# Kernel tuning notes

Hardware: AMD Instinct MI355X
Metric: run time of the kernel (lower is better)

The kernel has to match this reference:

```python
import jax, jax.numpy as jnp
import numpy as np

B, S, E, A = 4, 2048, 1024, 1024

def setup_inputs() -> dict:
    key = jax.random.key(0)
    ks = jax.random.split(key, 6)
    scale = 1.0 / np.sqrt(E)
    return {
        "query": jax.random.normal(ks[0], (B, S, E), jnp.float32),
        "key": jax.random.normal(ks[1], (B, S, E), jnp.float32),
        "value": jax.random.normal(ks[2], (B, S, E), jnp.float32),
        "Wq": jax.random.normal(ks[3], (E, A), jnp.float32) * scale,
        "bq": jnp.zeros((A,), jnp.float32),
        "Wk": jax.random.normal(ks[4], (E, A), jnp.float32) * scale,
        "bk": jnp.zeros((A,), jnp.float32),
        "Wv": jax.random.normal(ks[5], (E, A), jnp.float32) * scale,
        "bv": jnp.zeros((A,), jnp.float32),
    }

def reference(query, key, value, Wq, bq, Wk, bk, Wv, bv):
    # QKV linear projections: [B,S,E] @ [E,A] + [A]
    q = jnp.einsum("bse,ea->bsa", query, Wq) + bq
    k = jnp.einsum("bse,ea->bsa", key, Wk) + bk
    v = jnp.einsum("bse,ea->bsa", value, Wv) + bv
    # scaled dot-product attention (no mask, single head)
    inv_sqrt_d = 1.0 / jnp.sqrt(jnp.asarray(A, q.dtype))
    scores = jnp.einsum("bqa,bka->bqk", q, k) * inv_sqrt_d  # [B,S,S]
    probs = jax.nn.softmax(scores, axis=-1)
    return jnp.einsum("bqk,bka->bqa", probs, v)
```

## Files before the change

### kernel.cpp

```cpp
#include <hip/hip_runtime.h>

typedef unsigned short u16;
typedef __attribute__((ext_vector_type(4))) float f32x4;
typedef __attribute__((ext_vector_type(8))) short s16x8;
typedef __attribute__((ext_vector_type(8))) unsigned short u16x8;
typedef __attribute__((ext_vector_type(4))) unsigned short u16x4;

__device__ __forceinline__ u16 f2b(float x) {
  union { float f; unsigned u; } v; v.f = x;
  unsigned r = v.u + 0x7fffu + ((v.u >> 16) & 1u);
  return (u16)(r >> 16);
}
__device__ __forceinline__ float b2f(u16 x) {
  union { unsigned u; float f; } v; v.u = ((unsigned)x) << 16;
  return v.f;
}

__global__ __launch_bounds__(256) void cast3_f32_bf16(const float* __restrict__ s0,
                                                      const float* __restrict__ s1,
                                                      const float* __restrict__ s2,
                                                      u16* __restrict__ dst, long n4) {
  const float* src = (blockIdx.y == 0) ? s0 : ((blockIdx.y == 1) ? s1 : s2);
  long i = blockIdx.x * 256 + threadIdx.x;
  if (i >= n4) return;
  float4 f = ((const float4*)src)[i];
  u16x4 o;
  o.x = f2b(f.x); o.y = f2b(f.y); o.z = f2b(f.z); o.w = f2b(f.w);
  ((u16x4*)(dst + blockIdx.y * n4 * 4))[i] = o;
}

__global__ __launch_bounds__(256) void transpose_cast_w3(const float* __restrict__ w0,
                                                         const float* __restrict__ w1,
                                                         const float* __restrict__ w2,
                                                         u16* __restrict__ Wt, int E_, int A_) {
  __shared__ float tile[32][33];
  const float* W = (blockIdx.z == 0) ? w0 : ((blockIdx.z == 1) ? w1 : w2);
  u16* dst = Wt + (long)blockIdx.z * E_ * A_;
  int a0 = blockIdx.x * 32, e0 = blockIdx.y * 32;
  int tx = threadIdx.x & 31, ty = threadIdx.x >> 5;
  for (int i = ty; i < 32; i += 8) tile[i][tx] = W[(long)(e0 + i) * A_ + a0 + tx];
  __syncthreads();
  for (int i = ty; i < 32; i += 8) dst[(long)(a0 + i) * E_ + e0 + tx] = f2b(tile[tx][i]);
}

template<int BN, bool OUT_BF16>
__global__ __launch_bounds__(512, 2)
void gemmK32(const u16* __restrict__ Ag, const u16* __restrict__ Bg,
             const float* __restrict__ b0, const float* __restrict__ b1,
             const float* __restrict__ b2, void* __restrict__ Cg,
             int gn, int K, int N, float scale,
             long sA, long sB, long sC,
             u16* __restrict__ VtG, long vtB, int vtS) {
  constexpr int J = BN / 64;
  constexpr int WN = BN / 4;
  constexpr int OPS = 2 + BN / 128;
  constexpr int BUFSZ = (256 + BN) * 64;
  __shared__ __align__(128) char ldsc[4 * BUFSZ];

  const int t = threadIdx.x;
  const int w = t >> 6, l = t & 63;
  const int wm = w >> 2, wn = w & 3;

  const int nwg = gridDim.x;
  const int Lb = blockIdx.x;
  const int chunk = nwg >> 3;
  const int id = (Lb & 7) * chunk + (Lb >> 3);
  const int im = id / gn, in = id % gn;
  const int m0 = im * 256, n0 = in * BN;
  const int z = blockIdx.z;
  const float* bias = (z == 0) ? b0 : ((z == 1) ? b1 : b2);

  const u16* Ab = Ag + (long)z * sA + (long)m0 * K;
  const u16* Bb = Bg + (long)z * sB + (long)n0 * K;

  const long so0 = (long)(t >> 2) * K + (long)(((t & 3) ^ ((t >> 3) & 3)) << 3);
  const int d16 = t * 16;

  const int cbR = ((l >> 4) ^ ((l >> 1) & 3)) << 4;
  const int aB = (wm << 13) + ((l & 15) << 6) + cbR;
  const int bB = 16384 + wn * (WN * 64) + ((l & 15) << 6) + cbR;

  f32x4 acc[8][J] = {};
  s16x8 af[4], bf[J];
  const int NTt = K >> 5;

#define GLD(SRC, DST)                                                                        \
  __builtin_amdgcn_global_load_lds(                                                         \
      (const __attribute__((address_space(1))) unsigned int*)(SRC),                         \
      (__attribute__((address_space(3))) unsigned int*)(DST), 16, 0, 0)

#define STGA(TT) do {                                                                        \
    const u16* _s = Ab + ((long)(TT) << 5) + so0;                                            \
    char* _d = ldsc + ((TT) & 3) * BUFSZ + d16;                                              \
    GLD(_s, _d);                                                                             \
    GLD(_s + (long)128 * K, _d + 8192);                                                      \
  } while (0)

#define STGB(TT) do {                                                                        \
    const u16* _s = Bb + ((long)(TT) << 5) + so0;                                            \
    char* _d = ldsc + ((TT) & 3) * BUFSZ + 16384 + d16;                                      \
    GLD(_s, _d);                                                                             \
    if (BN == 256) GLD(_s + (long)128 * K, _d + 8192);                                       \
  } while (0)

  STGA(0); STGB(0); STGA(1); STGB(1); STGA(2); STGB(2);
  if (OPS == 4) asm volatile("s_waitcnt vmcnt(8)" ::: "memory");
  else          asm volatile("s_waitcnt vmcnt(6)" ::: "memory");
  __builtin_amdgcn_s_barrier();

  for (int tt = 0; tt < NTt; ++tt) {
    const int base = (tt & 3) * BUFSZ;
#pragma unroll
    for (int i = 0; i < 4; ++i) af[i] = *(const s16x8*)(ldsc + base + aB + (i << 10));
#pragma unroll
    for (int j = 0; j < J; ++j) bf[j] = *(const s16x8*)(ldsc + base + bB + (j << 10));
    if (tt + 3 < NTt) STGA(tt + 3);
    __builtin_amdgcn_s_setprio(1);
#pragma unroll
    for (int i = 0; i < 4; ++i)
#pragma unroll
      for (int j = 0; j < J; ++j)
        acc[i][j] = __builtin_amdgcn_mfma_f32_16x16x32_bf16(af[i], bf[j], acc[i][j], 0, 0, 0);
    __builtin_amdgcn_s_setprio(0);
    __builtin_amdgcn_s_barrier();

#pragma unroll
    for (int i = 0; i < 4; ++i) af[i] = *(const s16x8*)(ldsc + base + aB + 4096 + (i << 10));
    if (tt + 3 < NTt) STGB(tt + 3);
    __builtin_amdgcn_s_setprio(1);
#pragma unroll
    for (int i = 0; i < 4; ++i)
#pragma unroll
      for (int j = 0; j < J; ++j)
        acc[4 + i][j] = __builtin_amdgcn_mfma_f32_16x16x32_bf16(af[i], bf[j], acc[4 + i][j], 0, 0, 0);
    __builtin_amdgcn_s_setprio(0);
    if (tt <= NTt - 4) {
      if (OPS == 4) asm volatile("s_waitcnt vmcnt(8)" ::: "memory");
      else          asm volatile("s_waitcnt vmcnt(6)" ::: "memory");
    } else if (tt == NTt - 3) {
      if (OPS == 4) asm volatile("s_waitcnt vmcnt(4)" ::: "memory");
      else          asm volatile("s_waitcnt vmcnt(3)" ::: "memory");
    } else if (tt == NTt - 2) {
      asm volatile("s_waitcnt vmcnt(0)" ::: "memory");
    }
    __builtin_amdgcn_s_barrier();
  }
#undef STGA
#undef STGB
#undef GLD

  float bj[J];
#pragma unroll
  for (int j = 0; j < J; ++j) {
    int col = n0 + wn * WN + j * 16 + (l & 15);
    bj[j] = bias ? bias[col] : 0.0f;
  }

  if (OUT_BF16 && VtG != nullptr && z == 2) {
    const int b = m0 / vtS, smod = m0 % vtS;
    u16* vbase = VtG + (long)b * vtB + smod + wm * 128 + ((l >> 4) << 2);
#pragma unroll
    for (int i8 = 0; i8 < 8; ++i8)
#pragma unroll
      for (int j = 0; j < J; ++j) {
        int col = n0 + wn * WN + j * 16 + (l & 15);
        u16x4 o;
#pragma unroll
        for (int r = 0; r < 4; ++r) o[r] = f2b(acc[i8][j][r] * scale + bj[j]);
        *(u16x4*)(vbase + (long)col * vtS + i8 * 16) = o;
      }
  } else {
    long rbase = (long)z * sC + (long)(m0 + wm * 128 + ((l >> 4) << 2)) * N + n0 + wn * WN + (l & 15);
#pragma unroll
    for (int i8 = 0; i8 < 8; ++i8)
#pragma unroll
      for (int j = 0; j < J; ++j)
#pragma unroll
        for (int r = 0; r < 4; ++r) {
          float v = acc[i8][j][r] * scale + bj[j];
          long ro = rbase + (long)(i8 * 16 + r) * N + j * 16;
          if (OUT_BF16) ((u16*)Cg)[ro] = f2b(v);
          else          ((float*)Cg)[ro] = v;
        }
  }
}

__device__ __forceinline__ float wred_max(float x) {
  for (int o = 32; o > 0; o >>= 1) x = fmaxf(x, __shfl_xor(x, o));
  return x;
}
__device__ __forceinline__ float wred_sum(float x) {
  for (int o = 32; o > 0; o >>= 1) x += __shfl_xor(x, o);
  return x;
}

__global__ __launch_bounds__(256) void softmax_rows_bf16(const u16* __restrict__ S,
                                                         u16* __restrict__ P, int ncols) {
  long row = blockIdx.x;
  const u16x8* s8 = (const u16x8*)(S + row * (long)ncols);
  int t = threadIdx.x;
  int wave = t >> 6, lane = t & 63;
  u16x8 a = s8[t];
  float f[8];
#pragma unroll
  for (int i = 0; i < 8; i++) f[i] = b2f(a[i]);
  float m = f[0];
#pragma unroll
  for (int i = 1; i < 8; i++) m = fmaxf(m, f[i]);
  m = wred_max(m);
  __shared__ float redm[4], reds[4];
  if (lane == 0) redm[wave] = m;
  __syncthreads();
  m = fmaxf(fmaxf(redm[0], redm[1]), fmaxf(redm[2], redm[3]));

  float e[8], s = 0.f;
#pragma unroll
  for (int i = 0; i < 8; i++) { e[i] = __expf(f[i] - m); s += e[i]; }
  s = wred_sum(s);
  if (lane == 0) reds[wave] = s;
  __syncthreads();
  s = reds[0] + reds[1] + reds[2] + reds[3];
  float inv = 1.0f / s;

  u16x8 o;
#pragma unroll
  for (int i = 0; i < 8; i++) o[i] = f2b(e[i] * inv);
  ((u16x8*)(P + row * (long)ncols))[t] = o;
}

extern "C" void kernel_launch(void* const* d_in, const int* in_sizes, int n_in,
                              void* d_out, int out_size, void* d_ws, size_t ws_size,
                              hipStream_t stream) {
  const float* query = (const float*)d_in[0];
  const float* key_  = (const float*)d_in[1];
  const float* value = (const float*)d_in[2];
  const float* Wq = (const float*)d_in[3];
  const float* bq = (const float*)d_in[4];
  const float* Wk = (const float*)d_in[5];
  const float* bk = (const float*)d_in[6];
  const float* Wv = (const float*)d_in[7];
  const float* bv = (const float*)d_in[8];

  constexpr int B = 4, S = 2048, E = 1024, A = 1024;
  constexpr long MB = 1024 * 1024;
  char* ws = (char*)d_ws;
  u16* Qb  = (u16*)(ws + 0 * MB);
  u16* Kb  = (u16*)(ws + 16 * MB);
  u16* Vt  = (u16*)(ws + 48 * MB);
  u16* P   = (u16*)(ws + 64 * MB);
  u16* Sc  = (u16*)(ws + 96 * MB);
  u16* Xq  = (u16*)(ws + 96 * MB);
  u16* WqT = (u16*)(ws + 144 * MB);

  const long n = (long)B * S * E;
  const long n4 = n / 4;
  dim3 blk(256);

  cast3_f32_bf16<<<dim3(n4 / 256, 3), blk, 0, stream>>>(query, key_, value, Xq, n4);

  transpose_cast_w3<<<dim3(A / 32, E / 32, 3), blk, 0, stream>>>(Wq, Wk, Wv, WqT, E, A);

  gemmK32<256, true><<<dim3(128, 1, 3), dim3(512), 0, stream>>>(
      Xq, WqT, bq, bk, bv, Qb, 4, E, A, 1.0f,
      (long)8 * MB, (long)1 * MB, (long)8 * MB,
      Vt, (long)A * S, S);

  gemmK32<256, true><<<dim3(64, 1, 4), dim3(512), 0, stream>>>(
      Qb, Kb, nullptr, nullptr, nullptr, Sc, 8, A, S, 0.03125f,
      (long)S * A, (long)S * A, (long)S * S, nullptr, 0, 1);

  softmax_rows_bf16<<<dim3(B * S), blk, 0, stream>>>(Sc, P, S);

  gemmK32<128, false><<<dim3(64, 1, 4), dim3(512), 0, stream>>>(
      P, Vt, nullptr, nullptr, nullptr, (float*)d_out, 8, S, A, 1.0f,
      (long)S * S, (long)S * A, (long)S * A, nullptr, 0, 1);
}
```

Baseline: 312.9 us.

## Replace 8-wave GEMM with 4-wave 128x256 tile kernel and split-K for PV

Replaces the 512-thread, 256xBN-tile GEMM with a 256-thread kernel that computes 128x256 output tiles. It uses a three-stage LDS ring with one combined A+B stage load per K step, instead of four buffers with separate A and B halves. The P·V GEMM is split into two K halves written as fp32 partials into workspace, then summed by a new elementwise add kernel. The aim is more workgroups and better CU occupancy on every GEMM, at the cost of an extra pass over the fp32 partials and a different pipelining depth.

```diff
diff --git a/kernel.cpp b/kernel.cpp
--- a/kernel.cpp
+++ b/kernel.cpp
@@ -43,146 +43,134 @@
   for (int i = ty; i < 32; i += 8) dst[(long)(a0 + i) * E_ + e0 + tx] = f2b(tile[tx][i]);
 }
 
-template<int BN, bool OUT_BF16>
-__global__ __launch_bounds__(512, 2)
-void gemmK32(const u16* __restrict__ Ag, const u16* __restrict__ Bg,
-             const float* __restrict__ b0, const float* __restrict__ b1,
-             const float* __restrict__ b2, void* __restrict__ Cg,
-             int gn, int K, int N, float scale,
-             long sA, long sB, long sC,
-             u16* __restrict__ VtG, long vtB, int vtS) {
-  constexpr int J = BN / 64;
-  constexpr int WN = BN / 4;
-  constexpr int OPS = 2 + BN / 128;
-  constexpr int BUFSZ = (256 + BN) * 64;
-  __shared__ __align__(128) char ldsc[4 * BUFSZ];
-
+template<bool OUT_BF16, bool KSPLIT>
+__global__ __launch_bounds__(256, 2)
+void gemm4w(const u16* __restrict__ Ag, const u16* __restrict__ Bg,
+            const float* __restrict__ b0, const float* __restrict__ b1,
+            const float* __restrict__ b2, void* __restrict__ Cg,
+            int gn, int KLEN, int LDA, int LDB, int N, float scale,
+            long sA, long sB, long sC, long sKh,
+            u16* __restrict__ VtG, long vtB, int vtS) {
+  __shared__ __align__(128) char ldsc[73728];
   const int t = threadIdx.x;
   const int w = t >> 6, l = t & 63;
-  const int wm = w >> 2, wn = w & 3;
 
   const int nwg = gridDim.x;
   const int Lb = blockIdx.x;
   const int chunk = nwg >> 3;
   const int id = (Lb & 7) * chunk + (Lb >> 3);
   const int im = id / gn, in = id % gn;
-  const int m0 = im * 256, n0 = in * BN;
-  const int z = blockIdx.z;
+  const int m0 = im * 128, n0 = in * 256;
+  int z = blockIdx.z, kh = 0;
+  if (KSPLIT) { kh = z & 1; z >>= 1; }
   const float* bias = (z == 0) ? b0 : ((z == 1) ? b1 : b2);
 
-  const u16* Ab = Ag + (long)z * sA + (long)m0 * K;
-  const u16* Bb = Bg + (long)z * sB + (long)n0 * K;
-
-  const long so0 = (long)(t >> 2) * K + (long)(((t & 3) ^ ((t >> 3) & 3)) << 3);
+  const u16* Ab = Ag + (long)z * sA + (long)m0 * LDA + (long)kh * KLEN;
+  const u16* Bb = Bg + (long)z * sB + (long)n0 * LDB + (long)kh * KLEN;
+
+  const long soA = (long)(t >> 2) * LDA + (long)(((t & 3) ^ ((t >> 3) & 3)) << 3);
+  const long soB = (long)(t >> 2) * LDB + (long)(((t & 3) ^ ((t >> 3) & 3)) << 3);
   const int d16 = t * 16;
 
-  const int cbR = ((l >> 4) ^ ((l >> 1) & 3)) << 4;
-  const int aB = (wm << 13) + ((l & 15) << 6) + cbR;
-  const int bB = 16384 + wn * (WN * 64) + ((l & 15) << 6) + cbR;
-
-  f32x4 acc[8][J] = {};
-  s16x8 af[4], bf[J];
-  const int NTt = K >> 5;
+  const int cbR = (((l >> 4) ^ ((l >> 1) & 3)) << 4);
+  const int aB = ((l & 15) << 6) + cbR;
+  const int bB = 8192 + (w << 12) + ((l & 15) << 6) + cbR;
+
+  f32x4 acc[8][4] = {};
+  s16x8 af[8], bf[4];
+  const int NTt = KLEN >> 5;
 
 #define GLD(SRC, DST)                                                                        \
   __builtin_amdgcn_global_load_lds(                                                         \
       (const __attribute__((address_space(1))) unsigned int*)(SRC),                         \
       (__attribute__((address_space(3))) unsigned int*)(DST), 16, 0, 0)
 
-#define STGA(TT) do {                                                                        \
-    const u16* _s = Ab + ((long)(TT) << 5) + so0;                                            \
-    char* _d = ldsc + ((TT) & 3) * BUFSZ + d16;                                              \
-    GLD(_s, _d);                                                                             \
-    GLD(_s + (long)128 * K, _d + 8192);                                                      \
+#define STG(TT, SBASE) do {                                                                  \
+    const u16* _sa = Ab + ((long)(TT) << 5) + soA;                                           \
+    GLD(_sa,                   ldsc + (SBASE) + d16);                                        \
+    GLD(_sa + (long)64 * LDA,  ldsc + (SBASE) + 4096 + d16);                                 \
+    const u16* _sv = Bb + ((long)(TT) << 5) + soB;                                           \
+    GLD(_sv,                   ldsc + (SBASE) + 8192 + d16);                                 \
+    GLD(_sv + (long)64 * LDB,  ldsc + (SBASE) + 12288 + d16);                                \
+    GLD(_sv + (long)128 * LDB, ldsc + (SBASE) + 16384 + d16);                                \
+    GLD(_sv + (long)192 * LDB, ldsc + (SBASE) + 20480 + d16);                                \
   } while (0)
 
-#define STGB(TT) do {                                                                        \
-    const u16* _s = Bb + ((long)(TT) << 5) + so0;                                            \
-    char* _d = ldsc + ((TT) & 3) * BUFSZ + 16384 + d16;                                      \
-    GLD(_s, _d);                                                                             \
-    if (BN == 256) GLD(_s + (long)128 * K, _d + 8192);                                       \
-  } while (0)
-
-  STGA(0); STGB(0); STGA(1); STGB(1); STGA(2); STGB(2);
-  if (OPS == 4) asm volatile("s_waitcnt vmcnt(8)" ::: "memory");
-  else          asm volatile("s_waitcnt vmcnt(6)" ::: "memory");
+  STG(0, 0);
+  STG(1, 24576);
+  asm volatile("s_waitcnt vmcnt(6)" ::: "memory");
   __builtin_amdgcn_s_barrier();
 
+  int cb = 0, sb = 49152;
   for (int tt = 0; tt < NTt; ++tt) {
-    const int base = (tt & 3) * BUFSZ;
-#pragma unroll
-    for (int i = 0; i < 4; ++i) af[i] = *(const s16x8*)(ldsc + base + aB + (i << 10));
-#pragma unroll
-    for (int j = 0; j < J; ++j) bf[j] = *(const s16x8*)(ldsc + base + bB + (j << 10));
-    if (tt + 3 < NTt) STGA(tt + 3);
+#pragma unroll
+    for (int i = 0; i < 8; ++i) af[i] = *(const s16x8*)(ldsc + cb + aB + (i << 10));
+#pragma unroll
+    for (int j = 0; j < 4; ++j) bf[j] = *(const s16x8*)(ldsc + cb + bB + (j << 10));
+    if (tt + 2 < NTt) STG(tt + 2, sb);
     __builtin_amdgcn_s_setprio(1);
 #pragma unroll
-    for (int i = 0; i < 4; ++i)
-#pragma unroll
-      for (int j = 0; j < J; ++j)
+    for (int i = 0; i < 8; ++i)
+#pragma unroll
+      for (int j = 0; j < 4; ++j)
         acc[i][j] = __builtin_amdgcn_mfma_f32_16x16x32_bf16(af[i], bf[j], acc[i][j], 0, 0, 0);
     __builtin_amdgcn_s_setprio(0);
+    if (tt + 2 < NTt)      asm volatile("s_waitcnt vmcnt(6)" ::: "memory");
+    else if (tt + 1 < NTt) asm volatile("s_waitcnt vmcnt(0)" ::: "memory");
     __builtin_amdgcn_s_barrier();
-
-#pragma unroll
-    for (int i = 0; i < 4; ++i) af[i] = *(const s16x8*)(ldsc + base + aB + 4096 + (i << 10));
-    if (tt + 3 < NTt) STGB(tt + 3);
-    __builtin_amdgcn_s_setprio(1);
-#pragma unroll
-    for (int i = 0; i < 4; ++i)
-#pragma unroll
-      for (int j = 0; j < J; ++j)
-        acc[4 + i][j] = __builtin_amdgcn_mfma_f32_16x16x32_bf16(af[i], bf[j], acc[4 + i][j], 0, 0, 0);
-    __builtin_amdgcn_s_setprio(0);
-    if (tt <= NTt - 4) {
-      if (OPS == 4) asm volatile("s_waitcnt vmcnt(8)" ::: "memory");
-      else          asm volatile("s_waitcnt vmcnt(6)" ::: "memory");
-    } else if (tt == NTt - 3) {
-      if (OPS == 4) asm volatile("s_waitcnt vmcnt(4)" ::: "memory");
-      else          asm volatile("s_waitcnt vmcnt(3)" ::: "memory");
-    } else if (tt == NTt - 2) {
-      asm volatile("s_waitcnt vmcnt(0)" ::: "memory");
-    }
-    __builtin_amdgcn_s_barrier();
+    cb += 24576; if (cb >= 73728) cb = 0;
+    sb += 24576; if (sb >= 73728) sb = 0;
   }
-#undef STGA
-#undef STGB
+#undef STG
 #undef GLD
 
-  float bj[J];
-#pragma unroll
-  for (int j = 0; j < J; ++j) {
-    int col = n0 + wn * WN + j * 16 + (l & 15);
+  float bj[4];
+#pragma unroll
+  for (int j = 0; j < 4; ++j) {
+    int col = n0 + w * 64 + j * 16 + (l & 15);
     bj[j] = bias ? bias[col] : 0.0f;
   }
 
   if (OUT_BF16 && VtG != nullptr && z == 2) {
     const int b = m0 / vtS, smod = m0 % vtS;
-    u16* vbase = VtG + (long)b * vtB + smod + wm * 128 + ((l >> 4) << 2);
+    u16* vbase = VtG + (long)b * vtB + smod + ((l >> 4) << 2);
 #pragma unroll
     for (int i8 = 0; i8 < 8; ++i8)
 #pragma unroll
-      for (int j = 0; j < J; ++j) {
-        int col = n0 + wn * WN + j * 16 + (l & 15);
+      for (int j = 0; j < 4; ++j) {
+        int col = n0 + w * 64 + j * 16 + (l & 15);
         u16x4 o;
 #pragma unroll
         for (int r = 0; r < 4; ++r) o[r] = f2b(acc[i8][j][r] * scale + bj[j]);
         *(u16x4*)(vbase + (long)col * vtS + i8 * 16) = o;
       }
   } else {
-    long rbase = (long)z * sC + (long)(m0 + wm * 128 + ((l >> 4) << 2)) * N + n0 + wn * WN + (l & 15);
+    char* Cz = (char*)Cg;
+    long rbase = (long)z * sC + (KSPLIT ? (long)kh * sKh : 0) +
+                 (long)(m0 + ((l >> 4) << 2)) * N + n0 + w * 64 + (l & 15);
 #pragma unroll
     for (int i8 = 0; i8 < 8; ++i8)
 #pragma unroll
-      for (int j = 0; j < J; ++j)
+      for (int j = 0; j < 4; ++j)
 #pragma unroll
         for (int r = 0; r < 4; ++r) {
           float v = acc[i8][j][r] * scale + bj[j];
           long ro = rbase + (long)(i8 * 16 + r) * N + j * 16;
-          if (OUT_BF16) ((u16*)Cg)[ro] = f2b(v);
-          else          ((float*)Cg)[ro] = v;
+          if (OUT_BF16) ((u16*)Cz)[ro] = f2b(v);
+          else          ((float*)Cz)[ro] = v;
         }
   }
+}
+
+__global__ __launch_bounds__(256) void add2_f32(const float* __restrict__ a,
+                                                const float* __restrict__ b,
+                                                float* __restrict__ o, long n4) {
+  long i = blockIdx.x * 256 + threadIdx.x;
+  if (i >= n4) return;
+  float4 x = ((const float4*)a)[i];
+  float4 y = ((const float4*)b)[i];
+  float4 r; r.x = x.x + y.x; r.y = x.y + y.y; r.z = x.z + y.z; r.w = x.w + y.w;
+  ((float4*)o)[i] = r;
 }
 
 __device__ __forceinline__ float wred_max(float x) {
@@ -251,6 +239,7 @@
   u16* Sc  = (u16*)(ws + 96 * MB);
   u16* Xq  = (u16*)(ws + 96 * MB);
   u16* WqT = (u16*)(ws + 144 * MB);
+  float* Cp0 = (float*)(ws + 0 * MB);
 
   const long n = (long)B * S * E;
   const long n4 = n / 4;
@@ -260,18 +249,22 @@
 
   transpose_cast_w3<<<dim3(A / 32, E / 32, 3), blk, 0, stream>>>(Wq, Wk, Wv, WqT, E, A);
 
-  gemmK32<256, true><<<dim3(128, 1, 3), dim3(512), 0, stream>>>(
-      Xq, WqT, bq, bk, bv, Qb, 4, E, A, 1.0f,
-      (long)8 * MB, (long)1 * MB, (long)8 * MB,
+  gemm4w<true, false><<<dim3(256, 1, 3), blk, 0, stream>>>(
+      Xq, WqT, bq, bk, bv, Qb, 4, E, E, E, A, 1.0f,
+      (long)8 * MB, (long)1 * MB, (long)8 * MB, 0,
       Vt, (long)A * S, S);
 
-  gemmK32<256, true><<<dim3(64, 1, 4), dim3(512), 0, stream>>>(
-      Qb, Kb, nullptr, nullptr, nullptr, Sc, 8, A, S, 0.03125f,
-      (long)S * A, (long)S * A, (long)S * S, nullptr, 0, 1);
+  gemm4w<true, false><<<dim3(128, 1, 4), blk, 0, stream>>>(
+      Qb, Kb, nullptr, nullptr, nullptr, Sc, 8, A, A, A, S, 0.03125f,
+      (long)S * A, (long)S * A, (long)S * S, 0, nullptr, 0, 1);
 
   softmax_rows_bf16<<<dim3(B * S), blk, 0, stream>>>(Sc, P, S);
 
-  gemmK32<128, false><<<dim3(64, 1, 4), dim3(512), 0, stream>>>(
-      P, Vt, nullptr, nullptr, nullptr, (float*)d_out, 8, S, A, 1.0f,
-      (long)S * S, (long)S * A, (long)S * A, nullptr, 0, 1);
-}
+  gemm4w<false, true><<<dim3(64, 1, 8), blk, 0, stream>>>(
+      P, Vt, nullptr, nullptr, nullptr, Cp0, 4, 1024, S, S, A, 1.0f,
+      (long)S * S, (long)S * A, (long)S * A, (long)24 * MB, nullptr, 0, 1);
+
+  const long o4 = (long)B * S * A / 4;
+  add2_f32<<<dim3(o4 / 256), blk, 0, stream>>>(Cp0, (const float*)(ws + 96 * MB),
+                                               (float*)d_out, o4);
+}
```

New measurement: 320.7 us. 2.5% more time.
